# Optimization experiments

Hardware: AMD Instinct MI355X
Metric: run time of the kernel (lower is better)

Reference implementation:

```python
import math
import jax, jax.numpy as jnp
import numpy as np

LAM = 1.0
TAU = 0.0
BETA0 = -2.0 / (math.e + 0.08)  # lower clamp from the paper; 0.5*BETA0 > -1/e, so W is on the principal real branch


def lambertw(y, iters=8):
    """Principal-branch Lambert W via Halley iterations; valid for y > -1/e."""
    w = jnp.log1p(y)  # good initial guess for y > -1 (here y >= 0.5*BETA0 ~ -0.367)
    for _ in range(iters):
        e = jnp.exp(w)
        f = w * e - y
        w = w - f / (e * (w + 1.0) - (w + 2.0) * f / (2.0 * w + 2.0))
    return w


def bce_with_logits(pr, gt):
    # elementwise BCE with logits, reduction='none'
    return jnp.logaddexp(0.0, pr) - pr * gt


def setup_inputs() -> dict:
    key = jax.random.key(0)
    k1, k2 = jax.random.split(key)
    pr = jax.random.normal(k1, (32, 1, 1024, 1024), dtype=jnp.float32)
    gt = jax.random.uniform(k2, (32, 1, 1024, 1024), dtype=jnp.float32)
    return {"pr": pr, "gt": gt}


def reference(pr, gt):
    input_loss = bce_with_logits(pr, gt)
    beta = (input_loss - TAU) / LAM
    y = 0.5 * jnp.maximum(BETA0, beta)
    # scipy lambertw is outside the autograd graph in the original; sigma is a constant weight
    sigma = jax.lax.stop_gradient(jnp.exp(-lambertw(y)))
    loss = sigma * (input_loss - TAU) + LAM * jnp.log(sigma) ** 2
    return loss
```

## Files before the change

kernel.cpp:

```cpp
#include <hip/hip_runtime.h>
#include <math.h>


typedef float f32x4 __attribute__((ext_vector_type(4)));

__device__ __forceinline__ float superloss_elem(float pr, float gt) {
    const float LOG2E = 1.44269504f;
    const float LN2   = 0.69314718f;

    float t  = __builtin_amdgcn_exp2f(-fabsf(pr) * LOG2E);
    float lg = __builtin_amdgcn_logf(1.0f + t);
    float il = __fmaf_rn(-pr, gt, fmaxf(pr, 0.0f));
    il = __fmaf_rn(LN2, lg, il);

    float y   = 0.5f * il;
    float opy = 1.0f + y;
    float w0  = LN2 * __builtin_amdgcn_logf(opy);

    float f   = __fmaf_rn(w0, opy, -y);
    float wp1 = w0 + 1.0f;
    float num = 2.0f * f * wp1;
    float den = __fmaf_rn(opy + opy, wp1 * wp1, -(w0 + 2.0f) * f);
    float w1  = __fmaf_rn(-num, __builtin_amdgcn_rcpf(den), w0);

    float nd = w1 - w0;
    float p  = __fmaf_rn(nd, 0.041666668f, 0.16666667f);
    p = __fmaf_rn(nd, p, 0.5f);
    p = __fmaf_rn(nd, p, 1.0f);
    p = __fmaf_rn(nd, p, 1.0f);
    float e = opy * p;

    float f2 = __fmaf_rn(w1, e, -y);
    float d2 = e * (w1 + 1.0f);
    float w  = __fmaf_rn(-f2, __builtin_amdgcn_rcpf(d2), w1);

    float u = w + 1.0f;
    return __fmaf_rn(u, u, -1.0f);
}

__device__ __forceinline__ f32x4 superloss_vec(f32x4 p, f32x4 g) {
    f32x4 o;
    o.x = superloss_elem(p.x, g.x);
    o.y = superloss_elem(p.y, g.y);
    o.z = superloss_elem(p.z, g.z);
    o.w = superloss_elem(p.w, g.w);
    return o;
}

__global__ __launch_bounds__(256) void superloss_vec8(const f32x4* __restrict__ pr,
                                                      const f32x4* __restrict__ gt,
                                                      f32x4* __restrict__ out,
                                                      int n4) {
    int i0 = blockIdx.x * 512 + threadIdx.x;
    int i1 = i0 + 256;
    if (i1 < n4) {
        f32x4 p0 = pr[i0];
        f32x4 p1 = pr[i1];
        f32x4 g0 = gt[i0];
        f32x4 g1 = gt[i1];
        f32x4 o0 = superloss_vec(p0, g0);
        f32x4 o1 = superloss_vec(p1, g1);
        out[i0] = o0;
        out[i1] = o1;
    } else if (i0 < n4) {
        out[i0] = superloss_vec(pr[i0], gt[i0]);
    }
}

__global__ __launch_bounds__(256) void superloss_scalar(const float* __restrict__ pr,
                                                        const float* __restrict__ gt,
                                                        float* __restrict__ out,
                                                        int base, int n) {
    int i = base + blockIdx.x * blockDim.x + threadIdx.x;
    if (i < n) {
        out[i] = superloss_elem(pr[i], gt[i]);
    }
}

extern "C" void kernel_launch(void* const* d_in, const int* in_sizes, int n_in,
                              void* d_out, int out_size, void* d_ws, size_t ws_size,
                              hipStream_t stream) {
    const float* pr = (const float*)d_in[0];
    const float* gt = (const float*)d_in[1];
    float* out = (float*)d_out;
    int n = in_sizes[0];

    int n4 = n / 4;
    if (n4 > 0) {
        int blocks = (n4 + 511) / 512;
        superloss_vec8<<<blocks, 256, 0, stream>>>((const f32x4*)pr, (const f32x4*)gt,
                                                   (f32x4*)out, n4);
    }
    int rem = n - n4 * 4;
    if (rem > 0) {
        superloss_scalar<<<1, 256, 0, stream>>>(pr, gt, out, n4 * 4, n);
    }
}
```

Measured before the change: 305.0 us.

## Use persistent grid-stride loop with software-prefetched loads

Replaces the one-shot kernel, where each thread handled two vectors, with a persistent grid-stride kernel capped at 2048 blocks. Each iteration issues the loads for the next vector before computing and storing the current one, so memory latency overlaps with the transcendental math. It also cuts block launch overhead. The trade-off is fewer loads in flight per thread at a time and a small grid of 2048 blocks, which may not saturate HBM bandwidth on MI355X.

```diff
diff --git a/kernel.cpp b/kernel.cpp
--- a/kernel.cpp
+++ b/kernel.cpp
@@ -47,24 +47,27 @@
     return o;
 }
 
-__global__ __launch_bounds__(256) void superloss_vec8(const f32x4* __restrict__ pr,
+__global__ __launch_bounds__(256) void superloss_pipe(const f32x4* __restrict__ pr,
                                                       const f32x4* __restrict__ gt,
                                                       f32x4* __restrict__ out,
                                                       int n4) {
-    int i0 = blockIdx.x * 512 + threadIdx.x;
-    int i1 = i0 + 256;
-    if (i1 < n4) {
-        f32x4 p0 = pr[i0];
-        f32x4 p1 = pr[i1];
-        f32x4 g0 = gt[i0];
-        f32x4 g1 = gt[i1];
-        f32x4 o0 = superloss_vec(p0, g0);
-        f32x4 o1 = superloss_vec(p1, g1);
-        out[i0] = o0;
-        out[i1] = o1;
-    } else if (i0 < n4) {
-        out[i0] = superloss_vec(pr[i0], gt[i0]);
+    const int stride = gridDim.x * blockDim.x;
+    int idx = blockIdx.x * blockDim.x + threadIdx.x;
+    if (idx >= n4) return;
+
+    f32x4 pc = pr[idx];
+    f32x4 gc = gt[idx];
+    int nidx = idx + stride;
+    while (nidx < n4) {
+        f32x4 pn = pr[nidx];
+        f32x4 gn = gt[nidx];
+        out[idx] = superloss_vec(pc, gc);
+        pc = pn;
+        gc = gn;
+        idx = nidx;
+        nidx += stride;
     }
+    out[idx] = superloss_vec(pc, gc);
 }
 
 __global__ __launch_bounds__(256) void superloss_scalar(const float* __restrict__ pr,
@@ -87,8 +90,9 @@
 
     int n4 = n / 4;
     if (n4 > 0) {
-        int blocks = (n4 + 511) / 512;
-        superloss_vec8<<<blocks, 256, 0, stream>>>((const f32x4*)pr, (const f32x4*)gt,
+        int blocks = (n4 + 255) / 256;
+        if (blocks > 2048) blocks = 2048;
+        superloss_pipe<<<blocks, 256, 0, stream>>>((const f32x4*)pr, (const f32x4*)gt,
                                                    (f32x4*)out, n4);
     }
     int rem = n - n4 * 4;
```

Result: slower. 312.2 us (+2.3%).
